# Kernel tuning notes

Measured on AMD Instinct MI355X. Metric: run time of the kernel, lower is better.

## Reference

```python
import jax, jax.numpy as jnp
import numpy as np

B, R, L, D = 32, 48, 128, 64
PRIOR_HOURS = 48.0


def setup_inputs() -> dict:
    key = jax.random.key(0)
    ks = jax.random.split(key, 9)
    X = jax.random.normal(ks[0], (B, L, D), dtype=jnp.float32)
    # observation times in [0, prior_hours]
    T = jax.random.uniform(ks[1], (B, L, D), dtype=jnp.float32) * PRIOR_HOURS
    # observation mask (0/1 float, as used in the paper)
    M = (jax.random.uniform(ks[2], (B, L, D)) > 0.5).astype(jnp.float32)
    PD = jax.random.normal(ks[3], (B, L, D), dtype=jnp.float32)
    # learned parameters (glorot-uniform-like small init)
    alpha = jax.random.normal(ks[4], (R, 1, 1), dtype=jnp.float32) * 0.1
    w_v = jax.random.normal(ks[5], (R, L, D), dtype=jnp.float32) * 0.05
    w_t = jax.random.normal(ks[6], (R, L, D, 4), dtype=jnp.float32) * 0.05
    b_t = jax.random.normal(ks[7], (R, L, D, 1), dtype=jnp.float32) * 0.05
    b_v = jax.random.normal(ks[8], (R, 1, D), dtype=jnp.float32) * 0.05
    # fixed reference time grid (buffer, not trained)
    ref_time = jnp.linspace(0.0, PRIOR_HOURS, R, dtype=jnp.float32).reshape(R, 1, 1)
    return {"X": X, "T": T, "M": M, "PD": PD, "alpha": alpha,
            "w_v": w_v, "w_t": w_t, "b_t": b_t, "b_v": b_v, "ref_time": ref_time}


def reference(X, T, M, PD, alpha, w_v, w_t, b_t, b_v, ref_time):
    # broadcast over R ref time points instead of tf.tile: [B,R,L,D]
    dist = jnp.abs(T[:, None, :, :] - ref_time)          # type_distance == 'abs'
    kernel = jnp.exp(-jax.nn.relu(alpha) * dist)          # [B,R,L,D]
    intensity = jax.nn.relu(X[:, None, :, :] * kernel)    # [B,R,L,D]
    shp = dist.shape
    feats = jnp.stack([
        jnp.broadcast_to(X[:, None, :, :], shp),
        intensity,
        jnp.broadcast_to(M[:, None, :, :], shp),
        jnp.broadcast_to(PD[:, None, :, :], shp),
    ], axis=-1)                                            # [B,R,L,D,4] == tf.concat on axis 4
    # reduce_sum(w_t * feats + b_t, axis=4): broadcast b_t over the 4-axis -> 4*b_t
    latent = jax.nn.relu(jnp.einsum('rlde,brlde->brld', w_t, feats) + 4.0 * b_t[..., 0])
    # reduce_sum(w_v * latent + b_v, axis=2): b_v broadcast over L -> L*b_v
    out = jax.nn.relu(jnp.einsum('rld,brld->brd', w_v, latent) + L * b_v[:, 0, :])
    return out  # [B, R, D]
```

## Files before the change

### kernel.cpp

```cpp
#include <hip/hip_runtime.h>

#define B 32
#define R 48
#define L 128
#define D 64

template<int TR_, int TB_, int NS_>
__global__ __launch_bounds__(256) void alnn_part1_t(
    const float* __restrict__ X, const float* __restrict__ T,
    const float* __restrict__ M, const float* __restrict__ PD,
    const float* __restrict__ alpha, const float* __restrict__ w_v,
    const float* __restrict__ w_t, const float* __restrict__ b_t,
    const float* __restrict__ ref_time, float* __restrict__ ws)
{
    constexpr int NBT = B / TB_;
    constexpr int LCH = L / NS_;
    constexpr int LW  = LCH / 4;
    const int id   = blockIdx.x;
    const int s    = id % NS_;
    const int rest = id / NS_;
    const int bt   = rest % NBT;
    const int rt   = rest / NBT;
    const int d    = threadIdx.x & 63;
    const int ly   = threadIdx.x >> 6;
    const int r0 = rt * TR_, b0 = bt * TB_;

    float a_[TR_], rt_[TR_];
    #pragma unroll
    for (int r = 0; r < TR_; ++r) {
        a_[r]  = fmaxf(alpha[r0 + r], 0.0f);
        rt_[r] = ref_time[r0 + r];
    }

    float acc[TR_][TB_];
    #pragma unroll
    for (int r = 0; r < TR_; ++r)
        #pragma unroll
        for (int b = 0; b < TB_; ++b) acc[r][b] = 0.0f;

    const float4* __restrict__ w_t4 = reinterpret_cast<const float4*>(w_t);
    const int l0 = s * LCH + ly * LW;

    #pragma unroll
    for (int li = 0; li < LW; ++li) {
        const int l = l0 + li;
        float4 wt[TR_]; float btv[TR_], wv[TR_];
        #pragma unroll
        for (int r = 0; r < TR_; ++r) {
            const int iw = ((r0 + r) * L + l) * D + d;
            wt[r]  = w_t4[iw];
            btv[r] = 4.0f * b_t[iw];
            wv[r]  = w_v[iw];
        }
        float xv[TB_], tv[TB_], mv[TB_], pv[TB_];
        #pragma unroll
        for (int b = 0; b < TB_; ++b) {
            const int ix = ((b0 + b) * L + l) * D + d;
            xv[b] = X[ix];  tv[b] = T[ix];  mv[b] = M[ix];  pv[b] = PD[ix];
        }
        #pragma unroll
        for (int r = 0; r < TR_; ++r) {
            #pragma unroll
            for (int b = 0; b < TB_; ++b) {
                const float dist  = fabsf(tv[b] - rt_[r]);
                const float kern  = __expf(-a_[r] * dist);
                const float inten = fmaxf(xv[b] * kern, 0.0f);
                const float ssum  = fmaf(wt[r].x, xv[b],
                                    fmaf(wt[r].y, inten,
                                    fmaf(wt[r].z, mv[b],
                                    fmaf(wt[r].w, pv[b], btv[r]))));
                acc[r][b] = fmaf(wv[r], fmaxf(ssum, 0.0f), acc[r][b]);
            }
        }
    }

    __shared__ float red[4][TR_ * TB_][64];
    #pragma unroll
    for (int r = 0; r < TR_; ++r)
        #pragma unroll
        for (int b = 0; b < TB_; ++b)
            red[ly][r * TB_ + b][d] = acc[r][b];
    __syncthreads();

    #pragma unroll
    for (int p = ly; p < TR_ * TB_; p += 4) {
        const int r = p / TB_, b = p % TB_;
        const float v = red[0][p][d] + red[1][p][d] + red[2][p][d] + red[3][p][d];
        ws[(((size_t)s * B + (b0 + b)) * R + (r0 + r)) * D + d] = v;
    }
}

template<int NS_>
__global__ __launch_bounds__(256) void alnn_part2_t(
    const float* __restrict__ ws, const float* __restrict__ b_v,
    float* __restrict__ out)
{
    const int i = blockIdx.x * 256 + threadIdx.x;
    const int d = i & 63;
    const int r = (i >> 6) % R;
    const int b = i / (R * D);
    float sum = 0.0f;
    #pragma unroll
    for (int s = 0; s < NS_; ++s)
        sum += ws[(((size_t)s * B + b) * R + r) * D + d];
    out[i] = fmaxf(sum + (float)L * b_v[r * D + d], 0.0f);
}

__global__ __launch_bounds__(256) void alnn_fallback(
    const float* __restrict__ X, const float* __restrict__ T,
    const float* __restrict__ M, const float* __restrict__ PD,
    const float* __restrict__ alpha, const float* __restrict__ w_v,
    const float* __restrict__ w_t, const float* __restrict__ b_t,
    const float* __restrict__ b_v, const float* __restrict__ ref_time,
    float* __restrict__ out)
{
    const int br = blockIdx.x;
    const int b  = br / R;
    const int r  = br - b * R;
    const int d  = threadIdx.x & 63;
    const int ly = threadIdx.x >> 6;

    const float a  = fmaxf(alpha[r], 0.0f);
    const float rt = ref_time[r];
    const int baseX = b * L * D + d;
    const int baseW = r * L * D + d;

    float acc = 0.0f;
    const int l0 = ly * 32;
    #pragma unroll 4
    for (int li = 0; li < 32; ++li) {
        const int l  = l0 + li;
        const int ix = baseX + l * D;
        const int iw = baseW + l * D;
        const float x  = X[ix], t = T[ix], m = M[ix], pd = PD[ix];
        const float dist  = fabsf(t - rt);
        const float kern  = __expf(-a * dist);
        const float inten = fmaxf(x * kern, 0.0f);
        const float4 wt = reinterpret_cast<const float4*>(w_t)[iw];
        const float bt  = b_t[iw];
        float s = fmaf(wt.x, x, fmaf(wt.y, inten, fmaf(wt.z, m, fmaf(wt.w, pd, 4.0f * bt))));
        acc = fmaf(w_v[iw], fmaxf(s, 0.0f), acc);
    }
    __shared__ float red[4][64];
    red[ly][d] = acc;
    __syncthreads();
    if (ly == 0) {
        const float sum = red[0][d] + red[1][d] + red[2][d] + red[3][d];
        out[(b * R + r) * D + d] = fmaxf(sum + (float)L * b_v[r * D + d], 0.0f);
    }
}

extern "C" void kernel_launch(void* const* d_in, const int* in_sizes, int n_in,
                              void* d_out, int out_size, void* d_ws, size_t ws_size,
                              hipStream_t stream) {
    const float* X  = (const float*)d_in[0];
    const float* T  = (const float*)d_in[1];
    const float* M  = (const float*)d_in[2];
    const float* PD = (const float*)d_in[3];
    const float* alpha = (const float*)d_in[4];
    const float* w_v   = (const float*)d_in[5];
    const float* w_t   = (const float*)d_in[6];
    const float* b_t   = (const float*)d_in[7];
    const float* b_v   = (const float*)d_in[8];
    const float* ref_time = (const float*)d_in[9];
    float* out = (float*)d_out;
    float* ws  = (float*)d_ws;

    const size_t ws16 = (size_t)16 * B * R * D * sizeof(float);
    const size_t ws4  = (size_t) 4 * B * R * D * sizeof(float);

    if (ws_size >= ws16) {
        hipLaunchKernelGGL((alnn_part1_t<4, 4, 16>), dim3(1536), dim3(256), 0, stream,
                           X, T, M, PD, alpha, w_v, w_t, b_t, ref_time, ws);
        hipLaunchKernelGGL((alnn_part2_t<16>), dim3(B * R * D / 256), dim3(256), 0, stream,
                           ws, b_v, out);
    } else if (ws_size >= ws4) {
        hipLaunchKernelGGL((alnn_part1_t<2, 2, 4>), dim3(1536), dim3(256), 0, stream,
                           X, T, M, PD, alpha, w_v, w_t, b_t, ref_time, ws);
        hipLaunchKernelGGL((alnn_part2_t<4>), dim3(B * R * D / 256), dim3(256), 0, stream,
                           ws, b_v, out);
    } else {
        hipLaunchKernelGGL(alnn_fallback, dim3(B * R), dim3(256), 0, stream,
                           X, T, M, PD, alpha, w_v, w_t, b_t, b_v, ref_time, out);
    }
}
```

Before: 16.77 us.

## Split L across 32 slices, 2D-tile r/b per wave, pack observations into float4

```diff
diff --git a/kernel.cpp b/kernel.cpp
--- a/kernel.cpp
+++ b/kernel.cpp
@@ -4,6 +4,117 @@
 #define R 48
 #define L 128
 #define D 64
+
+__global__ __launch_bounds__(256) void alnn_prep(
+    const float* __restrict__ X, const float* __restrict__ T,
+    const float* __restrict__ M, const float* __restrict__ PD,
+    float4* __restrict__ obs4)
+{
+    const int i = blockIdx.x * 256 + threadIdx.x;
+    obs4[i] = make_float4(X[i], T[i], M[i], PD[i]);
+}
+
+template<int TRB, int TBB, int NS_, bool PACKED>
+__global__ __launch_bounds__(256) void alnn_part1_q(
+    const float* __restrict__ X, const float* __restrict__ T,
+    const float* __restrict__ M, const float* __restrict__ PD,
+    const float4* __restrict__ obs4,
+    const float* __restrict__ alpha, const float* __restrict__ w_v,
+    const float* __restrict__ w_t, const float* __restrict__ b_t,
+    const float* __restrict__ ref_time, float* __restrict__ ws)
+{
+    constexpr int TRW = TRB / 2;
+    constexpr int TBW = TBB / 2;
+    constexpr int NBT = B / TBB;
+    constexpr int LCH = L / NS_;
+
+    const int id   = blockIdx.x;
+    const int s    = id % NS_;
+    const int rest = id / NS_;
+    const int bt   = rest % NBT;
+    const int rt   = rest / NBT;
+
+    const int d  = threadIdx.x & 63;
+    const int ly = threadIdx.x >> 6;
+    const int r0 = rt * TRB + (ly >> 1) * TRW;
+    const int b0 = bt * TBB + (ly & 1) * TBW;
+
+    float a_[TRW], rt_[TRW];
+    #pragma unroll
+    for (int r = 0; r < TRW; ++r) {
+        a_[r]  = fmaxf(alpha[r0 + r], 0.0f);
+        rt_[r] = ref_time[r0 + r];
+    }
+
+    float acc[TRW][TBW];
+    #pragma unroll
+    for (int r = 0; r < TRW; ++r)
+        #pragma unroll
+        for (int b = 0; b < TBW; ++b) acc[r][b] = 0.0f;
+
+    const float4* __restrict__ w_t4 = reinterpret_cast<const float4*>(w_t);
+    const int l0 = s * LCH;
+
+    #pragma unroll
+    for (int li = 0; li < LCH; ++li) {
+        const int l = l0 + li;
+        float4 wt[TRW]; float btv[TRW], wv[TRW];
+        #pragma unroll
+        for (int r = 0; r < TRW; ++r) {
+            const int iw = ((r0 + r) * L + l) * D + d;
+            wt[r]  = w_t4[iw];
+            btv[r] = 4.0f * b_t[iw];
+            wv[r]  = w_v[iw];
+        }
+        float xv[TBW], tv[TBW], mv[TBW], pv[TBW];
+        #pragma unroll
+        for (int b = 0; b < TBW; ++b) {
+            const int ix = ((b0 + b) * L + l) * D + d;
+            if (PACKED) {
+                const float4 o = obs4[ix];
+                xv[b] = o.x; tv[b] = o.y; mv[b] = o.z; pv[b] = o.w;
+            } else {
+                xv[b] = X[ix]; tv[b] = T[ix]; mv[b] = M[ix]; pv[b] = PD[ix];
+            }
+        }
+        #pragma unroll
+        for (int r = 0; r < TRW; ++r) {
+            #pragma unroll
+            for (int b = 0; b < TBW; ++b) {
+                const float dist  = fabsf(tv[b] - rt_[r]);
+                const float kern  = __expf(-a_[r] * dist);
+                const float inten = fmaxf(xv[b] * kern, 0.0f);
+                const float ssum  = fmaf(wt[r].x, xv[b],
+                                    fmaf(wt[r].y, inten,
+                                    fmaf(wt[r].z, mv[b],
+                                    fmaf(wt[r].w, pv[b], btv[r]))));
+                acc[r][b] = fmaf(wv[r], fmaxf(ssum, 0.0f), acc[r][b]);
+            }
+        }
+    }
+
+    #pragma unroll
+    for (int r = 0; r < TRW; ++r)
+        #pragma unroll
+        for (int b = 0; b < TBW; ++b)
+            ws[(((size_t)s * B + (b0 + b)) * R + (r0 + r)) * D + d] = acc[r][b];
+}
+
+template<int NS_>
+__global__ __launch_bounds__(256) void alnn_part2_t(
+    const float* __restrict__ ws, const float* __restrict__ b_v,
+    float* __restrict__ out)
+{
+    const int i = blockIdx.x * 256 + threadIdx.x;
+    const int d = i & 63;
+    const int r = (i >> 6) % R;
+    const int b = i / (R * D);
+    float sum = 0.0f;
+    #pragma unroll
+    for (int s = 0; s < NS_; ++s)
+        sum += ws[(((size_t)s * B + b) * R + r) * D + d];
+    out[i] = fmaxf(sum + (float)L * b_v[r * D + d], 0.0f);
+}
 
 template<int TR_, int TB_, int NS_>
 __global__ __launch_bounds__(256) void alnn_part1_t(
@@ -31,7 +142,6 @@
         a_[r]  = fmaxf(alpha[r0 + r], 0.0f);
         rt_[r] = ref_time[r0 + r];
     }
-
     float acc[TR_][TB_];
     #pragma unroll
     for (int r = 0; r < TR_; ++r)
@@ -81,29 +191,12 @@
         for (int b = 0; b < TB_; ++b)
             red[ly][r * TB_ + b][d] = acc[r][b];
     __syncthreads();
-
     #pragma unroll
     for (int p = ly; p < TR_ * TB_; p += 4) {
         const int r = p / TB_, b = p % TB_;
         const float v = red[0][p][d] + red[1][p][d] + red[2][p][d] + red[3][p][d];
         ws[(((size_t)s * B + (b0 + b)) * R + (r0 + r)) * D + d] = v;
     }
-}
-
-template<int NS_>
-__global__ __launch_bounds__(256) void alnn_part2_t(
-    const float* __restrict__ ws, const float* __restrict__ b_v,
-    float* __restrict__ out)
-{
-    const int i = blockIdx.x * 256 + threadIdx.x;
-    const int d = i & 63;
-    const int r = (i >> 6) % R;
-    const int b = i / (R * D);
-    float sum = 0.0f;
-    #pragma unroll
-    for (int s = 0; s < NS_; ++s)
-        sum += ws[(((size_t)s * B + b) * R + r) * D + d];
-    out[i] = fmaxf(sum + (float)L * b_v[r * D + d], 0.0f);
 }
 
 __global__ __launch_bounds__(256) void alnn_fallback(
@@ -164,17 +257,35 @@
     const float* b_v   = (const float*)d_in[8];
     const float* ref_time = (const float*)d_in[9];
     float* out = (float*)d_out;
-    float* ws  = (float*)d_ws;
-
-    const size_t ws16 = (size_t)16 * B * R * D * sizeof(float);
-    const size_t ws4  = (size_t) 4 * B * R * D * sizeof(float);
-
-    if (ws_size >= ws16) {
+
+    const size_t part_bytes = (size_t)32 * B * R * D * sizeof(float);
+    const size_t obs_bytes  = (size_t)B * L * D * 4 * sizeof(float);
+    const size_t ws16       = (size_t)16 * B * R * D * sizeof(float);
+    const size_t ws4        = (size_t)4  * B * R * D * sizeof(float);
+
+    if (ws_size >= part_bytes + obs_bytes) {
+        float* ws   = (float*)d_ws;
+        float4* obs = (float4*)((char*)d_ws + part_bytes);
+        hipLaunchKernelGGL(alnn_prep, dim3(B * L * D / 256), dim3(256), 0, stream,
+                           X, T, M, PD, obs);
+        hipLaunchKernelGGL((alnn_part1_q<6, 8, 32, true>), dim3(1024), dim3(256), 0, stream,
+                           X, T, M, PD, obs, alpha, w_v, w_t, b_t, ref_time, ws);
+        hipLaunchKernelGGL((alnn_part2_t<32>), dim3(B * R * D / 256), dim3(256), 0, stream,
+                           ws, b_v, out);
+    } else if (ws_size >= part_bytes) {
+        float* ws = (float*)d_ws;
+        hipLaunchKernelGGL((alnn_part1_q<6, 8, 32, false>), dim3(1024), dim3(256), 0, stream,
+                           X, T, M, PD, nullptr, alpha, w_v, w_t, b_t, ref_time, ws);
+        hipLaunchKernelGGL((alnn_part2_t<32>), dim3(B * R * D / 256), dim3(256), 0, stream,
+                           ws, b_v, out);
+    } else if (ws_size >= ws16) {
+        float* ws = (float*)d_ws;
         hipLaunchKernelGGL((alnn_part1_t<4, 4, 16>), dim3(1536), dim3(256), 0, stream,
                            X, T, M, PD, alpha, w_v, w_t, b_t, ref_time, ws);
         hipLaunchKernelGGL((alnn_part2_t<16>), dim3(B * R * D / 256), dim3(256), 0, stream,
                            ws, b_v, out);
     } else if (ws_size >= ws4) {
+        float* ws = (float*)d_ws;
         hipLaunchKernelGGL((alnn_part1_t<2, 2, 4>), dim3(1536), dim3(256), 0, stream,
                            X, T, M, PD, alpha, w_v, w_t, b_t, ref_time, ws);
         hipLaunchKernelGGL((alnn_part2_t<4>), dim3(B * R * D / 256), dim3(256), 0, stream,
```

Measured after the change: 25.43 us. 1.52x slower.
